# Kernel tuning notes

Hardware: AMD Instinct MI355X
Metric: run time of the kernel (lower is better)

Reference implementation:

```python
import jax, jax.numpy as jnp
import numpy as np

B, N, E = 256, 128, 262144
LABEL_DIM, MAX_DEGREE, RW_DIM = 29, 16, 16
F = 128
NUM_LABELS = LABEL_DIM + MAX_DEGREE + RW_DIM  # 61
SK_ITER, SK_TAU = 6, 1.0


def _edges(k):
    k1, k2, k3 = jax.random.split(k, 3)
    g = jax.random.randint(k1, (E,), 0, B)
    src = g * N + jax.random.randint(k2, (E,), 0, N)
    dst = g * N + jax.random.randint(k3, (E,), 0, N)
    return src, dst


def setup_inputs():
    key = jax.random.key(0)
    ks = jax.random.split(key, 20)
    ntot = B * N
    s = 0.05
    nrm = lambda k, shp: jax.random.normal(k, shp, dtype=jnp.float32) * s
    src1, dst1 = _edges(ks[3])
    src2, dst2 = _edges(ks[7])
    return {
        'x1': jax.random.uniform(ks[0], (ntot, LABEL_DIM), dtype=jnp.float32),
        'cent1': jax.random.randint(ks[1], (ntot,), 0, MAX_DEGREE),
        'rw1': jax.random.uniform(ks[2], (ntot, RW_DIM), dtype=jnp.float32),
        'src1': src1, 'dst1': dst1,
        'x2': jax.random.uniform(ks[4], (ntot, LABEL_DIM), dtype=jnp.float32),
        'cent2': jax.random.randint(ks[5], (ntot,), 0, MAX_DEGREE),
        'rw2': jax.random.uniform(ks[6], (ntot, RW_DIM), dtype=jnp.float32),
        'src2': src2, 'dst2': dst2,
        'degree_emb': nrm(ks[8], (MAX_DEGREE, MAX_DEGREE)),
        'init_W': nrm(ks[9], (NUM_LABELS, F)), 'init_b': jnp.zeros((F,), jnp.float32),
        'W1': nrm(ks[10], (F, F)), 'b1': jnp.zeros((F,), jnp.float32),
        'W2': nrm(ks[11], (F, F)), 'b2': jnp.zeros((F,), jnp.float32),
        'W3': nrm(ks[12], (F, F)), 'b3': jnp.zeros((F,), jnp.float32),
        'A_aff': nrm(ks[13], (F, F)) + jnp.eye(F, dtype=jnp.float32),
        'sc_W1': nrm(ks[14], (8 * F, 64)), 'sc_b1': jnp.zeros((64,), jnp.float32),
        'sc_W2': nrm(ks[15], (64, 1)), 'sc_b2': jnp.zeros((1,), jnp.float32),
        'topk': 8,
    }


def gcn_conv(x, W, b, src, dst):
    # GCNConv: x' = D^{-1/2} (A + I) D^{-1/2} x W + b
    n = x.shape[0]
    h = x @ W
    loops = jnp.arange(n)
    s = jnp.concatenate([src, loops])
    d = jnp.concatenate([dst, loops])
    deg = jax.ops.segment_sum(jnp.ones_like(d, dtype=h.dtype), d, n)
    dinv = jax.lax.rsqrt(jnp.maximum(deg, 1.0))
    w = dinv[s] * dinv[d]
    return jax.ops.segment_sum(h[s] * w[:, None], d, n) + b


def conv_pass(feat, src, dst, W1, b1, W2, b2, W3, b3):
    f1 = gcn_conv(feat, W1, b1, src, dst)
    f2 = gcn_conv(jax.nn.relu(f1), W2, b2, src, dst)
    f3 = gcn_conv(jax.nn.relu(f2), W3, b3, src, dst)
    return f1, f2, f3


def affinity(xa, xb, A):
    Xa = xa.reshape(B, N, -1)
    Xb = xb.reshape(B, N, -1)
    return jnp.einsum('bif,fg,bjg->bij', Xa, A, Xb)


def soft_topk(scores, ks_tgt, n_iter, tau):
    # Entropic-OT soft top-k (Xie et al.) over flattened affinity entries vs 2 anchors,
    # normalized by SK_ITER log-domain Sinkhorn iterations.
    b, n, m = scores.shape
    L = n * m
    x = scores.reshape(b, L)
    a_lo = x.min(axis=1, keepdims=True) - 1.0
    a_hi = x.max(axis=1, keepdims=True) + 1.0
    anchors = jnp.concatenate([a_lo, a_hi], axis=1)      # [b, 2]
    logK = -jnp.abs(x[:, :, None] - anchors[:, None, :]) / tau  # [b, L, 2]
    log_mu = jnp.full((b, L), -jnp.log(float(L)), dtype=x.dtype)
    k = ks_tgt[:, None]
    nu = jnp.concatenate([(L - k) / L, k / L], axis=1)   # [b, 2]
    log_nu = jnp.log(nu)

    def body(carry, _):
        f, g = carry
        f = log_mu - jax.nn.logsumexp(logK + g[:, None, :], axis=2)
        g = log_nu - jax.nn.logsumexp(logK + f[:, :, None], axis=1)
        return (f, g), None

    init = (jnp.zeros((b, L), x.dtype), jnp.zeros((b, 2), x.dtype))
    (f, g), _ = jax.lax.scan(body, init, None, length=n_iter)
    gamma = jnp.exp(logK + f[:, :, None] + g[:, None, :])
    prob = (gamma[:, :, 1] * L).reshape(b, n, m)
    return gamma, prob


def reference(x1, cent1, rw1, src1, dst1, x2, cent2, rw2, src2, dst2,
              degree_emb, init_W, init_b, W1, b1, W2, b2, W3, b3, A_aff,
              sc_W1, sc_b1, sc_W2, sc_b2, topk):
    feat1 = jax.nn.relu(jnp.concatenate([x1, degree_emb[cent1], rw1], axis=1) @ init_W + init_b)
    feat2 = jax.nn.relu(jnp.concatenate([x2, degree_emb[cent2], rw2], axis=1) @ init_W + init_b)
    f11, f12, f13 = conv_pass(feat1, src1, dst1, W1, b1, W2, b2, W3, b3)
    f21, f22, f23 = conv_pass(feat2, src2, dst2, W1, b1, W2, b2, W3, b3)

    gt_ks = jnp.full((B,), topk / 2.0, dtype=feat1.dtype)
    _, sim1 = soft_topk(affinity(feat1, feat2, A_aff), gt_ks, SK_ITER, SK_TAU)
    _, sim2 = soft_topk(affinity(f13, f23, A_aff), gt_ks, SK_ITER, SK_TAU)

    gf1 = jnp.concatenate([feat1, f11, f12, f13], axis=1).reshape(B, N, -1).sum(axis=1)   # global_add_pool
    gf2 = jnp.concatenate([feat2, f21, f22, f23], axis=1).reshape(B, N, -1).max(axis=1)   # global_max_pool
    scores = jnp.concatenate([gf1, gf2], axis=1)  # [B, 8F]
    h = jax.nn.relu(scores @ sc_W1 + sc_b1)
    ged = jax.nn.sigmoid((h @ sc_W2 + sc_b2).reshape(-1))
    return ged, sim1, sim2
```

## Files before the change

kernel.cpp:

```cpp
#include <hip/hip_runtime.h>
#include <math.h>

#define BATCH 256
#define NNODE 128
#define NT    32768
#define FDIM  128
#define NEDGE 262144
#define LBL   29
#define MAXDEG 16
#define RWD   16
#define NTF   (NT * FDIM)

__global__ void k_zero2(int* __restrict__ p1, int* __restrict__ p2) {
  int i = blockIdx.x * 256 + threadIdx.x;
  if (i < NT) p1[i] = 0;
  else if (i < 2 * NT) p2[i - NT] = 0;
}
__global__ void k_deg2(const int* __restrict__ dst1, const int* __restrict__ dst2,
                       int* __restrict__ d1, int* __restrict__ d2) {
  int e = blockIdx.x * 256 + threadIdx.x;
  if (e < NEDGE) atomicAdd(&d1[dst1[e]], 1);
  else if (e < 2 * NEDGE) atomicAdd(&d2[dst2[e - NEDGE]], 1);
}
__global__ void k_dinv2(const int* __restrict__ d1, const int* __restrict__ d2,
                        float* __restrict__ v1, float* __restrict__ v2) {
  int i = blockIdx.x * 256 + threadIdx.x;
  if (i < NT) v1[i] = rsqrtf((float)(d1[i] + 1));
  else if (i < 2 * NT) v2[i - NT] = rsqrtf((float)(d2[i - NT] + 1));
}
__global__ __launch_bounds__(1024) void k_scan2(const int* __restrict__ degi1,
                                                int* __restrict__ ofs1, int* __restrict__ cur1,
                                                const int* __restrict__ degi2,
                                                int* __restrict__ ofs2, int* __restrict__ cur2) {
  const int* degi = blockIdx.x ? degi2 : degi1;
  int* ofs = blockIdx.x ? ofs2 : ofs1;
  int* cur = blockIdx.x ? cur2 : cur1;
  __shared__ int part[1024];
  int t = threadIdx.x;
  int base = t * 32;
  int loc[32]; int sum = 0;
#pragma unroll
  for (int u = 0; u < 32; ++u) { loc[u] = sum; sum += degi[base + u]; }
  part[t] = sum;
  __syncthreads();
  for (int off = 1; off < 1024; off <<= 1) {
    int v = (t >= off) ? part[t - off] : 0;
    __syncthreads();
    part[t] += v;
    __syncthreads();
  }
  int excl = (t == 0) ? 0 : part[t - 1];
#pragma unroll
  for (int u = 0; u < 32; ++u) {
    int o = excl + loc[u];
    ofs[base + u] = o; cur[base + u] = o;
  }
}
__global__ void k_fill2(const int* __restrict__ src1, const int* __restrict__ dst1,
                        int* __restrict__ cur1, int* __restrict__ csr1,
                        const int* __restrict__ src2, const int* __restrict__ dst2,
                        int* __restrict__ cur2, int* __restrict__ csr2) {
  int e = blockIdx.x * 256 + threadIdx.x;
  if (e < NEDGE) {
    int pos = atomicAdd(&cur1[dst1[e]], 1);
    csr1[pos] = src1[e];
  } else if (e < 2 * NEDGE) {
    e -= NEDGE;
    int pos = atomicAdd(&cur2[dst2[e]], 1);
    csr2[pos] = src2[e];
  }
}

__global__ __launch_bounds__(256, 2) void k_chain(
    const float* __restrict__ x1, const int* __restrict__ cent1, const float* __restrict__ rw1,
    const float* __restrict__ x2, const int* __restrict__ cent2, const float* __restrict__ rw2,
    const float* __restrict__ demb,
    const float* __restrict__ initW, const float* __restrict__ initb,
    const float* __restrict__ W1, const float* __restrict__ b1,
    const float* __restrict__ W2, const float* __restrict__ b2,
    const float* __restrict__ W3, const float* __restrict__ b3,
    const int* __restrict__ ofs1, const int* __restrict__ end1, const int* __restrict__ csr1,
    const int* __restrict__ ofs2, const int* __restrict__ end2, const int* __restrict__ csr2,
    const float* __restrict__ dinv1, const float* __restrict__ dinv2,
    float* __restrict__ feat1G, float* __restrict__ feat2G,
    float* __restrict__ f13G, float* __restrict__ f23G,
    float* __restrict__ gfs) {
  __shared__ float X[128 * 132];
  __shared__ float WcB[16 * 132];
  __shared__ float dvL[128];
  __shared__ float bL[128];
  __shared__ int   oL[128], enL[128];

  const int t = threadIdx.x;
  const int side = blockIdx.x >> 8;
  const int g = blockIdx.x & 255;
  const int nb = g * NNODE;

  const float* xg    = side ? x2 : x1;
  const int*   centg = side ? cent2 : cent1;
  const float* rwg   = side ? rw2 : rw1;
  const int*   ofsg  = side ? ofs2 : ofs1;
  const int*   endg  = side ? end2 : end1;
  const int*   csrg  = side ? csr2 : csr1;
  const float* dinvg = side ? dinv2 : dinv1;
  float* featG = side ? feat2G : feat1G;
  float* f3G   = side ? f23G : f13G;

  const int e_base = ofsg[nb];
  if (t < 128) {
    dvL[t] = dinvg[nb + t];
    oL[t]  = ofsg[nb + t] - e_base;
    enL[t] = endg[nb + t] - e_base;
  }
  {
    int d = t >> 1, sub = t & 1;
    int node = nb + d;
    int ct = centg[node];
    const float* xr = xg + (size_t)node * LBL;
    const float* er = demb + ct * MAXDEG;
    const float* rr = rwg + (size_t)node * RWD;
    for (int c = sub * 34; c < sub * 34 + 34; ++c) {
      float v = 0.f;
      if (c < LBL) v = xr[c];
      else if (c < LBL + MAXDEG) v = er[c - LBL];
      else if (c < 61) v = rr[c - 45];
      X[d * 68 + c] = v;
    }
  }
  __syncthreads();

  const int rg = t >> 3;
  const int jq = (t & 7) * 4;

  {
    float acc[4][16] = {};
    for (int kc = 0; kc < 64; kc += 16) {
      __syncthreads();
#pragma unroll
      for (int u = 0; u < 2; ++u) {
        int ll = t + 256 * u;
        int row = ll >> 5, c4 = (ll & 31) * 4;
        int gk = kc + row;
        float4 w = (gk < 61) ? *reinterpret_cast<const float4*>(&initW[(size_t)gk * FDIM + c4])
                             : make_float4(0.f, 0.f, 0.f, 0.f);
        *reinterpret_cast<float4*>(&WcB[row * 132 + c4]) = w;
      }
      if (kc == 0 && t < 128) bL[t] = initb[t];
      __syncthreads();
      for (int kk = 0; kk < 16; kk += 4) {
        float av[4][4];
#pragma unroll
        for (int r = 0; r < 4; ++r) {
          float4 tmp = *reinterpret_cast<const float4*>(&X[(rg + 32 * r) * 68 + kc + kk]);
          av[r][0] = tmp.x; av[r][1] = tmp.y; av[r][2] = tmp.z; av[r][3] = tmp.w;
        }
#pragma unroll
        for (int c = 0; c < 4; ++c) {
          float4 w0 = *reinterpret_cast<const float4*>(&WcB[(kk + c) * 132 + jq]);
          float4 w1 = *reinterpret_cast<const float4*>(&WcB[(kk + c) * 132 + 32 + jq]);
          float4 w2 = *reinterpret_cast<const float4*>(&WcB[(kk + c) * 132 + 64 + jq]);
          float4 w3 = *reinterpret_cast<const float4*>(&WcB[(kk + c) * 132 + 96 + jq]);
#pragma unroll
          for (int r = 0; r < 4; ++r) {
            float a = av[r][c];
            acc[r][0]  += a * w0.x; acc[r][1]  += a * w0.y; acc[r][2]  += a * w0.z; acc[r][3]  += a * w0.w;
            acc[r][4]  += a * w1.x; acc[r][5]  += a * w1.y; acc[r][6]  += a * w1.z; acc[r][7]  += a * w1.w;
            acc[r][8]  += a * w2.x; acc[r][9]  += a * w2.y; acc[r][10] += a * w2.z; acc[r][11] += a * w2.w;
            acc[r][12] += a * w3.x; acc[r][13] += a * w3.y; acc[r][14] += a * w3.z; acc[r][15] += a * w3.w;
          }
        }
      }
    }
    __syncthreads();
#pragma unroll
    for (int r = 0; r < 4; ++r) {
      int row = rg + 32 * r;
#pragma unroll
      for (int q = 0; q < 4; ++q) {
        int col = q * 32 + jq;
        float4 bl = *reinterpret_cast<const float4*>(&bL[col]);
        float4 o = make_float4(fmaxf(acc[r][q * 4 + 0] + bl.x, 0.f),
                               fmaxf(acc[r][q * 4 + 1] + bl.y, 0.f),
                               fmaxf(acc[r][q * 4 + 2] + bl.z, 0.f),
                               fmaxf(acc[r][q * 4 + 3] + bl.w, 0.f));
        *reinterpret_cast<float4*>(&X[row * 132 + col]) = o;
        *reinterpret_cast<float4*>(&featG[(size_t)(nb + row) * FDIM + col]) = o;
      }
    }
    __syncthreads();
  }

#define POOL_LAYER(layer)                                                            \
  {                                                                                  \
    int j4 = (t & 31) * 4, qq = t >> 5;                                              \
    float4 pv = side ? make_float4(-INFINITY, -INFINITY, -INFINITY, -INFINITY)       \
                     : make_float4(0.f, 0.f, 0.f, 0.f);                              \
    for (int r = 0; r < 16; ++r) {                                                   \
      float4 fv = *reinterpret_cast<const float4*>(&X[(qq * 16 + r) * 132 + j4]);    \
      if (side) { pv.x = fmaxf(pv.x, fv.x); pv.y = fmaxf(pv.y, fv.y);                \
                  pv.z = fmaxf(pv.z, fv.z); pv.w = fmaxf(pv.w, fv.w); }              \
      else      { pv.x += fv.x; pv.y += fv.y; pv.z += fv.z; pv.w += fv.w; }          \
    }                                                                                \
    *reinterpret_cast<float4*>(&WcB[qq * 128 + j4]) = pv;                            \
    __syncthreads();                                                                 \
    if (t < 128) {                                                                   \
      float v = side ? -INFINITY : 0.f;                                              \
      for (int q2 = 0; q2 < 8; ++q2) {                                               \
        float w2 = WcB[q2 * 128 + t];                                                \
        v = side ? fmaxf(v, w2) : (v + w2);                                          \
      }                                                                              \
      gfs[g * 1024 + side * 512 + (layer) * 128 + t] = v;                            \
    }                                                                                \
  }

  POOL_LAYER(0)

  for (int l = 0; l < 3; ++l) {
    const float* Wg = (l == 0) ? W1 : (l == 1) ? W2 : W3;
    const float* bg = (l == 0) ? b1 : (l == 1) ? b2 : b3;
    float acc[4][16] = {};
    for (int kc = 0; kc < 128; kc += 16) {
      __syncthreads();
#pragma unroll
      for (int u = 0; u < 2; ++u) {
        int ll = t + 256 * u;
        int row = ll >> 5, c4 = (ll & 31) * 4;
        *reinterpret_cast<float4*>(&WcB[row * 132 + c4]) =
            *reinterpret_cast<const float4*>(&Wg[(size_t)(kc + row) * FDIM + c4]);
      }
      if (kc == 0 && t < 128) bL[t] = bg[t];
      __syncthreads();
      for (int kk = 0; kk < 16; kk += 4) {
        float av[4][4];
#pragma unroll
        for (int r = 0; r < 4; ++r) {
          float4 tmp = *reinterpret_cast<const float4*>(&X[(rg + 32 * r) * 132 + kc + kk]);
          if (l > 0) {
            tmp.x = fmaxf(tmp.x, 0.f); tmp.y = fmaxf(tmp.y, 0.f);
            tmp.z = fmaxf(tmp.z, 0.f); tmp.w = fmaxf(tmp.w, 0.f);
          }
          av[r][0] = tmp.x; av[r][1] = tmp.y; av[r][2] = tmp.z; av[r][3] = tmp.w;
        }
#pragma unroll
        for (int c = 0; c < 4; ++c) {
          float4 w0 = *reinterpret_cast<const float4*>(&WcB[(kk + c) * 132 + jq]);
          float4 w1 = *reinterpret_cast<const float4*>(&WcB[(kk + c) * 132 + 32 + jq]);
          float4 w2 = *reinterpret_cast<const float4*>(&WcB[(kk + c) * 132 + 64 + jq]);
          float4 w3 = *reinterpret_cast<const float4*>(&WcB[(kk + c) * 132 + 96 + jq]);
#pragma unroll
          for (int r = 0; r < 4; ++r) {
            float a = av[r][c];
            acc[r][0]  += a * w0.x; acc[r][1]  += a * w0.y; acc[r][2]  += a * w0.z; acc[r][3]  += a * w0.w;
            acc[r][4]  += a * w1.x; acc[r][5]  += a * w1.y; acc[r][6]  += a * w1.z; acc[r][7]  += a * w1.w;
            acc[r][8]  += a * w2.x; acc[r][9]  += a * w2.y; acc[r][10] += a * w2.z; acc[r][11] += a * w2.w;
            acc[r][12] += a * w3.x; acc[r][13] += a * w3.y; acc[r][14] += a * w3.z; acc[r][15] += a * w3.w;
          }
        }
      }
    }
    __syncthreads();
#pragma unroll
    for (int r = 0; r < 4; ++r) {
      int row = rg + 32 * r;
#pragma unroll
      for (int q = 0; q < 4; ++q) {
        int col = q * 32 + jq;
        *reinterpret_cast<float4*>(&X[row * 132 + col]) =
            make_float4(acc[r][q * 4 + 0], acc[r][q * 4 + 1],
                        acc[r][q * 4 + 2], acc[r][q * 4 + 3]);
      }
    }
    __syncthreads();

    {
      int d = t >> 1, fc = (t & 1) * 64;
      float dd = dvL[d];
      float4 a[16];
#pragma unroll
      for (int u = 0; u < 16; ++u) {
        float4 hv = *reinterpret_cast<const float4*>(&X[d * 132 + fc + u * 4]);
        a[u] = make_float4(dd * hv.x, dd * hv.y, dd * hv.z, dd * hv.w);
      }
      int o0 = oL[d], o1 = enL[d];
      int sj = (o0 < o1) ? (csrg[e_base + o0] - nb) : 0;
      for (int j = o0; j < o1; ++j) {
        int sn = (j + 1 < o1) ? (csrg[e_base + j + 1] - nb) : 0;
        float w = dvL[sj];
#pragma unroll
        for (int u = 0; u < 16; ++u) {
          float4 hv = *reinterpret_cast<const float4*>(&X[sj * 132 + fc + u * 4]);
          a[u].x += w * hv.x; a[u].y += w * hv.y; a[u].z += w * hv.z; a[u].w += w * hv.w;
        }
        sj = sn;
      }
      __syncthreads();
#pragma unroll
      for (int u = 0; u < 16; ++u) {
        float4 bl = *reinterpret_cast<const float4*>(&bL[fc + u * 4]);
        float4 o = make_float4(bl.x + dd * a[u].x, bl.y + dd * a[u].y,
                               bl.z + dd * a[u].z, bl.w + dd * a[u].w);
        *reinterpret_cast<float4*>(&X[d * 132 + fc + u * 4]) = o;
        if (l == 2)
          *reinterpret_cast<float4*>(&f3G[(size_t)(nb + d) * FDIM + fc + u * 4]) = o;
      }
    }
    __syncthreads();

    POOL_LAYER(l + 1)
  }
#undef POOL_LAYER
}

__global__ __launch_bounds__(1024) void k_sim(const float* __restrict__ F1,
                                              const float* __restrict__ F2,
                                              const float* __restrict__ Aaff,
                                              const int* __restrict__ topk,
                                              float* __restrict__ Sout) {
  __shared__ float X1[128 * 132];
  __shared__ float X2[128 * 132];
  __shared__ float WcB[16 * 132];
  __shared__ float rA[16], rB[16], bc[2];

  const int t = threadIdx.x;
  const int b = blockIdx.x;
  const float* F1b = F1 + (size_t)b * NNODE * FDIM;
  const float* F2b = F2 + (size_t)b * NNODE * FDIM;

#pragma unroll
  for (int p = 0; p < 4; ++p) {
    int fi = t + 1024 * p;
    int row = fi >> 5, c4 = (fi & 31) * 4;
    *reinterpret_cast<float4*>(&X1[row * 132 + c4]) =
        *reinterpret_cast<const float4*>(&F1b[(size_t)row * FDIM + c4]);
    *reinterpret_cast<float4*>(&X2[row * 132 + c4]) =
        *reinterpret_cast<const float4*>(&F2b[(size_t)row * FDIM + c4]);
  }

  const int rg = t >> 3;
  const int jq = (t & 7) * 4;

  float acc[16];
#pragma unroll
  for (int u = 0; u < 16; ++u) acc[u] = 0.f;

  for (int kc = 0; kc < 128; kc += 16) {
    __syncthreads();
    if (t < 512) {
      int row = t >> 5, c4 = (t & 31) * 4;
      *reinterpret_cast<float4*>(&WcB[row * 132 + c4]) =
          *reinterpret_cast<const float4*>(&Aaff[(size_t)(kc + row) * FDIM + c4]);
    }
    __syncthreads();
    for (int kk = 0; kk < 16; kk += 4) {
      float4 a4 = *reinterpret_cast<const float4*>(&X1[rg * 132 + kc + kk]);
      float av[4] = {a4.x, a4.y, a4.z, a4.w};
#pragma unroll
      for (int c = 0; c < 4; ++c) {
        float4 w0 = *reinterpret_cast<const float4*>(&WcB[(kk + c) * 132 + jq]);
        float4 w1 = *reinterpret_cast<const float4*>(&WcB[(kk + c) * 132 + 32 + jq]);
        float4 w2 = *reinterpret_cast<const float4*>(&WcB[(kk + c) * 132 + 64 + jq]);
        float4 w3 = *reinterpret_cast<const float4*>(&WcB[(kk + c) * 132 + 96 + jq]);
        float a = av[c];
        acc[0]  += a * w0.x; acc[1]  += a * w0.y; acc[2]  += a * w0.z; acc[3]  += a * w0.w;
        acc[4]  += a * w1.x; acc[5]  += a * w1.y; acc[6]  += a * w1.z; acc[7]  += a * w1.w;
        acc[8]  += a * w2.x; acc[9]  += a * w2.y; acc[10] += a * w2.z; acc[11] += a * w2.w;
        acc[12] += a * w3.x; acc[13] += a * w3.y; acc[14] += a * w3.z; acc[15] += a * w3.w;
      }
    }
  }
  __syncthreads();
#pragma unroll
  for (int q = 0; q < 4; ++q)
    *reinterpret_cast<float4*>(&X1[rg * 132 + 32 * q + jq]) =
        make_float4(acc[q * 4 + 0], acc[q * 4 + 1], acc[q * 4 + 2], acc[q * 4 + 3]);

#pragma unroll
  for (int u = 0; u < 16; ++u) acc[u] = 0.f;

  for (int kc = 0; kc < 128; kc += 16) {
    __syncthreads();
#pragma unroll
    for (int p = 0; p < 2; ++p) {
      int id = t + 1024 * p;
      int kkr = id >> 7, c = id & 127;
      WcB[kkr * 132 + c] = X2[c * 132 + kc + kkr];
    }
    __syncthreads();
    for (int kk = 0; kk < 16; kk += 4) {
      float4 a4 = *reinterpret_cast<const float4*>(&X1[rg * 132 + kc + kk]);
      float av[4] = {a4.x, a4.y, a4.z, a4.w};
#pragma unroll
      for (int c = 0; c < 4; ++c) {
        float4 w0 = *reinterpret_cast<const float4*>(&WcB[(kk + c) * 132 + jq]);
        float4 w1 = *reinterpret_cast<const float4*>(&WcB[(kk + c) * 132 + 32 + jq]);
        float4 w2 = *reinterpret_cast<const float4*>(&WcB[(kk + c) * 132 + 64 + jq]);
        float4 w3 = *reinterpret_cast<const float4*>(&WcB[(kk + c) * 132 + 96 + jq]);
        float a = av[c];
        acc[0]  += a * w0.x; acc[1]  += a * w0.y; acc[2]  += a * w0.z; acc[3]  += a * w0.w;
        acc[4]  += a * w1.x; acc[5]  += a * w1.y; acc[6]  += a * w1.z; acc[7]  += a * w1.w;
        acc[8]  += a * w2.x; acc[9]  += a * w2.y; acc[10] += a * w2.z; acc[11] += a * w2.w;
        acc[12] += a * w3.x; acc[13] += a * w3.y; acc[14] += a * w3.z; acc[15] += a * w3.w;
      }
    }
  }

  const int wave = t >> 6, lane = t & 63;
  {
    float mn = acc[0], mx = acc[0];
#pragma unroll
    for (int u = 1; u < 16; ++u) { mn = fminf(mn, acc[u]); mx = fmaxf(mx, acc[u]); }
    for (int off = 32; off; off >>= 1) {
      mn = fminf(mn, __shfl_down(mn, off));
      mx = fmaxf(mx, __shfl_down(mx, off));
    }
    if (lane == 0) { rA[wave] = mn; rB[wave] = mx; }
    __syncthreads();
    if (t < 16) {
      mn = rA[t]; mx = rB[t];
      for (int off = 8; off; off >>= 1) {
        mn = fminf(mn, __shfl_down(mn, off));
        mx = fmaxf(mx, __shfl_down(mx, off));
      }
      if (t == 0) { bc[0] = mn - 1.f; bc[1] = mx + 1.f; }
    }
    __syncthreads();
  }
  float a_lo = bc[0], a_hi = bc[1];

  float p[16], q[16];
#pragma unroll
  for (int u = 0; u < 16; ++u) {
    p[u] = __expf(a_lo - acc[u]);
    q[u] = __expf(acc[u] - a_hi);
  }

  const float Lf = (float)(NNODE * NNODE);
  float kt = 0.5f * (float)topk[0];

  float E0 = 1.f, E1 = 1.f, E0p = 1.f, E1p = 1.f;
  for (int it = 0; it < 6; ++it) {
    E0p = E0; E1p = E1;
    float r0 = 0.f, r1 = 0.f;
#pragma unroll
    for (int u = 0; u < 16; ++u) {
      float denom = fmaf(p[u], E0, q[u] * E1);
      float rin = __builtin_amdgcn_rcpf(denom);
      r0 = fmaf(p[u], rin, r0);
      r1 = fmaf(q[u], rin, r1);
    }
    for (int off = 32; off; off >>= 1) {
      r0 += __shfl_down(r0, off);
      r1 += __shfl_down(r1, off);
    }
    if (lane == 0) { rA[wave] = r0; rB[wave] = r1; }
    __syncthreads();
    if (t < 16) {
      r0 = rA[t]; r1 = rB[t];
      for (int off = 8; off; off >>= 1) {
        r0 += __shfl_down(r0, off);
        r1 += __shfl_down(r1, off);
      }
      if (t == 0) { bc[0] = (Lf - kt) / r0; bc[1] = kt / r1; }
    }
    __syncthreads();
    E0 = bc[0]; E1 = bc[1];
    __syncthreads();
  }

  float* xrow = Sout + (size_t)b * NNODE * NNODE + (size_t)rg * NNODE;
#pragma unroll
  for (int qd = 0; qd < 4; ++qd) {
    float o[4];
#pragma unroll
    for (int j = 0; j < 4; ++j) {
      int u = qd * 4 + j;
      float denom = fmaf(p[u], E0p, q[u] * E1p);
      o[j] = q[u] * E1 * __builtin_amdgcn_rcpf(denom);
    }
    *reinterpret_cast<float4*>(&xrow[32 * qd + jq]) = make_float4(o[0], o[1], o[2], o[3]);
  }
}

__global__ __launch_bounds__(256) void k_mlp(const float* __restrict__ gfs,
                                             const float* __restrict__ W1,
                                             const float* __restrict__ b1,
                                             const float* __restrict__ W2,
                                             const float* __restrict__ b2,
                                             float* __restrict__ ged) {
  __shared__ float sm[1024];
  int b = blockIdx.x, t = threadIdx.x;
  const float* s = gfs + b * 1024;
#pragma unroll
  for (int qq = 0; qq < 4; ++qq) sm[t + 256 * qq] = s[t + 256 * qq];
  __syncthreads();
  int j4 = (t & 15) * 4, kp = t >> 4;
  float4 acc = make_float4(0.f, 0.f, 0.f, 0.f);
#pragma unroll 8
  for (int k = 0; k < 64; ++k) {
    float4 w = *reinterpret_cast<const float4*>(&W1[(size_t)(kp * 64 + k) * 64 + j4]);
    float sv = sm[kp * 64 + k];
    acc.x += sv * w.x; acc.y += sv * w.y; acc.z += sv * w.z; acc.w += sv * w.w;
  }
  __syncthreads();
  *reinterpret_cast<float4*>(&sm[kp * 64 + j4]) = acc;
  __syncthreads();
  if (t < 64) {
    float h = b1[t];
#pragma unroll
    for (int kp2 = 0; kp2 < 16; ++kp2) h += sm[kp2 * 64 + t];
    h = fmaxf(h, 0.f);
    float v = h * W2[t];
    for (int off = 32; off; off >>= 1) v += __shfl_down(v, off);
    if (t == 0) ged[b] = 1.f / (1.f + __expf(-(v + b2[0])));
  }
}

extern "C" void kernel_launch(void* const* d_in, const int* in_sizes, int n_in,
                              void* d_out, int out_size, void* d_ws, size_t ws_size,
                              hipStream_t stream) {
  (void)in_sizes; (void)n_in; (void)out_size; (void)ws_size;
  const float* x1    = (const float*)d_in[0];
  const int*   cent1 = (const int*)  d_in[1];
  const float* rw1   = (const float*)d_in[2];
  const int*   src1  = (const int*)  d_in[3];
  const int*   dst1  = (const int*)  d_in[4];
  const float* x2    = (const float*)d_in[5];
  const int*   cent2 = (const int*)  d_in[6];
  const float* rw2   = (const float*)d_in[7];
  const int*   src2  = (const int*)  d_in[8];
  const int*   dst2  = (const int*)  d_in[9];
  const float* demb  = (const float*)d_in[10];
  const float* initW = (const float*)d_in[11];
  const float* initb = (const float*)d_in[12];
  const float* W1    = (const float*)d_in[13];
  const float* b1    = (const float*)d_in[14];
  const float* W2    = (const float*)d_in[15];
  const float* b2    = (const float*)d_in[16];
  const float* W3    = (const float*)d_in[17];
  const float* b3    = (const float*)d_in[18];
  const float* Aaff  = (const float*)d_in[19];
  const float* scW1  = (const float*)d_in[20];
  const float* scb1  = (const float*)d_in[21];
  const float* scW2  = (const float*)d_in[22];
  const float* scb2  = (const float*)d_in[23];
  const int*   topk  = (const int*)  d_in[24];

  float* ws    = (float*)d_ws;
  float* feat1 = ws;
  float* feat2 = ws + (size_t)1 * NTF;
  float* f13   = ws + (size_t)2 * NTF;
  float* f23   = ws + (size_t)3 * NTF;
  float* dinv1 = ws + (size_t)4 * NTF;
  float* dinv2 = dinv1 + NT;
  float* gfs   = dinv2 + NT;

  float* ged = (float*)d_out;
  float* S1  = ged + BATCH;
  float* S2  = S1 + (size_t)BATCH * NNODE * NNODE;

  int* degi1 = (int*)S1;
  int* ofs1  = degi1 + NT;
  int* cur1  = ofs1 + NT;
  int* csr1  = cur1 + NT;
  int* degi2 = csr1 + NEDGE;
  int* ofs2  = degi2 + NT;
  int* cur2  = ofs2 + NT;
  int* csr2  = cur2 + NT;

  const int gE = NEDGE / 256;
  const int gN = NT / 256;

  k_zero2<<<2 * gN, 256, 0, stream>>>(degi1, degi2);
  k_deg2<<<2 * gE, 256, 0, stream>>>(dst1, dst2, degi1, degi2);
  k_dinv2<<<2 * gN, 256, 0, stream>>>(degi1, degi2, dinv1, dinv2);
  k_scan2<<<2, 1024, 0, stream>>>(degi1, ofs1, cur1, degi2, ofs2, cur2);
  k_fill2<<<2 * gE, 256, 0, stream>>>(src1, dst1, cur1, csr1, src2, dst2, cur2, csr2);

  k_chain<<<512, 256, 0, stream>>>(
      x1, cent1, rw1, x2, cent2, rw2, demb, initW, initb,
      W1, b1, W2, b2, W3, b3,
      ofs1, cur1, csr1, ofs2, cur2, csr2, dinv1, dinv2,
      feat1, feat2, f13, f23, gfs);

  k_mlp<<<BATCH, 256, 0, stream>>>(gfs, scW1, scb1, scW2, scb2, ged);

  k_sim<<<BATCH, 1024, 0, stream>>>(feat1, feat2, Aaff, topk, S1);
  k_sim<<<BATCH, 1024, 0, stream>>>(f13, f23, Aaff, topk, S2);
}
```

Baseline: 455.5 us.

## Prefetch weights into registers, merge sim launches, transpose X2 once, fuse dinv into scan

Register-prefetches the next weight tile in the chain and sim GEMM loops so global loads overlap the current tile's compute. The two k_sim launches become one 512-block launch. X2 is stored transposed with a rotated column offset at load time, which removes the per-tile transpose into WcB and its two barriers. The dinv computation moves into the scan kernel and the zero kernel becomes hipMemsetAsync, cutting launches at the cost of a slightly heavier single-block scan.

```diff
diff --git a/kernel.cpp b/kernel.cpp
--- a/kernel.cpp
+++ b/kernel.cpp
@@ -11,36 +11,32 @@
 #define RWD   16
 #define NTF   (NT * FDIM)
 
-__global__ void k_zero2(int* __restrict__ p1, int* __restrict__ p2) {
-  int i = blockIdx.x * 256 + threadIdx.x;
-  if (i < NT) p1[i] = 0;
-  else if (i < 2 * NT) p2[i - NT] = 0;
-}
 __global__ void k_deg2(const int* __restrict__ dst1, const int* __restrict__ dst2,
                        int* __restrict__ d1, int* __restrict__ d2) {
   int e = blockIdx.x * 256 + threadIdx.x;
   if (e < NEDGE) atomicAdd(&d1[dst1[e]], 1);
   else if (e < 2 * NEDGE) atomicAdd(&d2[dst2[e - NEDGE]], 1);
 }
-__global__ void k_dinv2(const int* __restrict__ d1, const int* __restrict__ d2,
-                        float* __restrict__ v1, float* __restrict__ v2) {
-  int i = blockIdx.x * 256 + threadIdx.x;
-  if (i < NT) v1[i] = rsqrtf((float)(d1[i] + 1));
-  else if (i < 2 * NT) v2[i - NT] = rsqrtf((float)(d2[i - NT] + 1));
-}
 __global__ __launch_bounds__(1024) void k_scan2(const int* __restrict__ degi1,
                                                 int* __restrict__ ofs1, int* __restrict__ cur1,
+                                                float* __restrict__ dinv1,
                                                 const int* __restrict__ degi2,
-                                                int* __restrict__ ofs2, int* __restrict__ cur2) {
+                                                int* __restrict__ ofs2, int* __restrict__ cur2,
+                                                float* __restrict__ dinv2) {
   const int* degi = blockIdx.x ? degi2 : degi1;
-  int* ofs = blockIdx.x ? ofs2 : ofs1;
-  int* cur = blockIdx.x ? cur2 : cur1;
+  int* ofs   = blockIdx.x ? ofs2  : ofs1;
+  int* cur   = blockIdx.x ? cur2  : cur1;
+  float* dnv = blockIdx.x ? dinv2 : dinv1;
   __shared__ int part[1024];
   int t = threadIdx.x;
   int base = t * 32;
   int loc[32]; int sum = 0;
 #pragma unroll
-  for (int u = 0; u < 32; ++u) { loc[u] = sum; sum += degi[base + u]; }
+  for (int u = 0; u < 32; ++u) {
+    int dg = degi[base + u];
+    loc[u] = sum; sum += dg;
+    dnv[base + u] = rsqrtf((float)(dg + 1));
+  }
   part[t] = sum;
   __syncthreads();
   for (int off = 1; off < 1024; off <<= 1) {
@@ -131,21 +127,32 @@
 
   const int rg = t >> 3;
   const int jq = (t & 7) * 4;
+  const int prow = t >> 5;
+  const int pc4  = (t & 31) * 4;
 
   {
     float acc[4][16] = {};
+    float4 wpre[2];
+#pragma unroll
+    for (int u = 0; u < 2; ++u) {
+      int gk = prow + 8 * u;
+      wpre[u] = (gk < 61) ? *reinterpret_cast<const float4*>(&initW[(size_t)gk * FDIM + pc4])
+                          : make_float4(0.f, 0.f, 0.f, 0.f);
+    }
     for (int kc = 0; kc < 64; kc += 16) {
       __syncthreads();
 #pragma unroll
-      for (int u = 0; u < 2; ++u) {
-        int ll = t + 256 * u;
-        int row = ll >> 5, c4 = (ll & 31) * 4;
-        int gk = kc + row;
-        float4 w = (gk < 61) ? *reinterpret_cast<const float4*>(&initW[(size_t)gk * FDIM + c4])
-                             : make_float4(0.f, 0.f, 0.f, 0.f);
-        *reinterpret_cast<float4*>(&WcB[row * 132 + c4]) = w;
-      }
+      for (int u = 0; u < 2; ++u)
+        *reinterpret_cast<float4*>(&WcB[(prow + 8 * u) * 132 + pc4]) = wpre[u];
       if (kc == 0 && t < 128) bL[t] = initb[t];
+      if (kc + 16 < 64) {
+#pragma unroll
+        for (int u = 0; u < 2; ++u) {
+          int gk = kc + 16 + prow + 8 * u;
+          wpre[u] = (gk < 61) ? *reinterpret_cast<const float4*>(&initW[(size_t)gk * FDIM + pc4])
+                              : make_float4(0.f, 0.f, 0.f, 0.f);
+        }
+      }
       __syncthreads();
       for (int kk = 0; kk < 16; kk += 4) {
         float av[4][4];
@@ -219,16 +226,21 @@
     const float* Wg = (l == 0) ? W1 : (l == 1) ? W2 : W3;
     const float* bg = (l == 0) ? b1 : (l == 1) ? b2 : b3;
     float acc[4][16] = {};
+    float4 wpre[2];
+#pragma unroll
+    for (int u = 0; u < 2; ++u)
+      wpre[u] = *reinterpret_cast<const float4*>(&Wg[(size_t)(prow + 8 * u) * FDIM + pc4]);
     for (int kc = 0; kc < 128; kc += 16) {
       __syncthreads();
 #pragma unroll
-      for (int u = 0; u < 2; ++u) {
-        int ll = t + 256 * u;
-        int row = ll >> 5, c4 = (ll & 31) * 4;
-        *reinterpret_cast<float4*>(&WcB[row * 132 + c4]) =
-            *reinterpret_cast<const float4*>(&Wg[(size_t)(kc + row) * FDIM + c4]);
-      }
+      for (int u = 0; u < 2; ++u)
+        *reinterpret_cast<float4*>(&WcB[(prow + 8 * u) * 132 + pc4]) = wpre[u];
       if (kc == 0 && t < 128) bL[t] = bg[t];
+      if (kc + 16 < 128) {
+#pragma unroll
+        for (int u = 0; u < 2; ++u)
+          wpre[u] = *reinterpret_cast<const float4*>(&Wg[(size_t)(kc + 16 + prow + 8 * u) * FDIM + pc4]);
+      }
       __syncthreads();
       for (int kk = 0; kk < 16; kk += 4) {
         float av[4][4];
@@ -311,20 +323,25 @@
 #undef POOL_LAYER
 }
 
-__global__ __launch_bounds__(1024) void k_sim(const float* __restrict__ F1,
-                                              const float* __restrict__ F2,
+__global__ __launch_bounds__(1024) void k_sim(const float* __restrict__ F1s1,
+                                              const float* __restrict__ F2s1,
+                                              const float* __restrict__ F1s2,
+                                              const float* __restrict__ F2s2,
                                               const float* __restrict__ Aaff,
                                               const int* __restrict__ topk,
-                                              float* __restrict__ Sout) {
+                                              float* __restrict__ S1,
+                                              float* __restrict__ S2) {
   __shared__ float X1[128 * 132];
   __shared__ float X2[128 * 132];
   __shared__ float WcB[16 * 132];
   __shared__ float rA[16], rB[16], bc[2];
 
   const int t = threadIdx.x;
-  const int b = blockIdx.x;
-  const float* F1b = F1 + (size_t)b * NNODE * FDIM;
-  const float* F2b = F2 + (size_t)b * NNODE * FDIM;
+  const int half = blockIdx.x >> 8;
+  const int b = blockIdx.x & 255;
+  const float* F1b = (half ? F1s2 : F1s1) + (size_t)b * NNODE * FDIM;
+  const float* F2b = (half ? F2s2 : F2s1) + (size_t)b * NNODE * FDIM;
+  float* Sout = (half ? S2 : S1) + (size_t)b * NNODE * NNODE;
 
 #pragma unroll
   for (int p = 0; p < 4; ++p) {
@@ -332,8 +349,12 @@
     int row = fi >> 5, c4 = (fi & 31) * 4;
     *reinterpret_cast<float4*>(&X1[row * 132 + c4]) =
         *reinterpret_cast<const float4*>(&F1b[(size_t)row * FDIM + c4]);
-    *reinterpret_cast<float4*>(&X2[row * 132 + c4]) =
-        *reinterpret_cast<const float4*>(&F2b[(size_t)row * FDIM + c4]);
+    float4 v = *reinterpret_cast<const float4*>(&F2b[(size_t)row * FDIM + c4]);
+    int ro = (row + c4) & 127;
+    X2[(c4 + 0) * 132 + ro] = v.x;
+    X2[(c4 + 1) * 132 + ro] = v.y;
+    X2[(c4 + 2) * 132 + ro] = v.z;
+    X2[(c4 + 3) * 132 + ro] = v.w;
   }
 
   const int rg = t >> 3;
@@ -343,12 +364,18 @@
 #pragma unroll
   for (int u = 0; u < 16; ++u) acc[u] = 0.f;
 
+  float4 apre;
+  if (t < 512) {
+    int row = t >> 5, c4 = (t & 31) * 4;
+    apre = *reinterpret_cast<const float4*>(&Aaff[(size_t)row * FDIM + c4]);
+  }
   for (int kc = 0; kc < 128; kc += 16) {
     __syncthreads();
     if (t < 512) {
       int row = t >> 5, c4 = (t & 31) * 4;
-      *reinterpret_cast<float4*>(&WcB[row * 132 + c4]) =
-          *reinterpret_cast<const float4*>(&Aaff[(size_t)(kc + row) * FDIM + c4]);
+      *reinterpret_cast<float4*>(&WcB[row * 132 + c4]) = apre;
+      if (kc + 16 < 128)
+        apre = *reinterpret_cast<const float4*>(&Aaff[(size_t)(kc + 16 + row) * FDIM + c4]);
     }
     __syncthreads();
     for (int kk = 0; kk < 16; kk += 4) {
@@ -376,25 +403,21 @@
 
 #pragma unroll
   for (int u = 0; u < 16; ++u) acc[u] = 0.f;
+  __syncthreads();
 
   for (int kc = 0; kc < 128; kc += 16) {
-    __syncthreads();
-#pragma unroll
-    for (int p = 0; p < 2; ++p) {
-      int id = t + 1024 * p;
-      int kkr = id >> 7, c = id & 127;
-      WcB[kkr * 132 + c] = X2[c * 132 + kc + kkr];
-    }
-    __syncthreads();
     for (int kk = 0; kk < 16; kk += 4) {
       float4 a4 = *reinterpret_cast<const float4*>(&X1[rg * 132 + kc + kk]);
       float av[4] = {a4.x, a4.y, a4.z, a4.w};
 #pragma unroll
       for (int c = 0; c < 4; ++c) {
-        float4 w0 = *reinterpret_cast<const float4*>(&WcB[(kk + c) * 132 + jq]);
-        float4 w1 = *reinterpret_cast<const float4*>(&WcB[(kk + c) * 132 + 32 + jq]);
-        float4 w2 = *reinterpret_cast<const float4*>(&WcB[(kk + c) * 132 + 64 + jq]);
-        float4 w3 = *reinterpret_cast<const float4*>(&WcB[(kk + c) * 132 + 96 + jq]);
+        int ck = kc + kk + c;
+        const float* xb = &X2[ck * 132];
+        int o0 = (jq + (ck & 124)) & 127;
+        float4 w0 = *reinterpret_cast<const float4*>(&xb[o0]);
+        float4 w1 = *reinterpret_cast<const float4*>(&xb[(o0 + 32) & 127]);
+        float4 w2 = *reinterpret_cast<const float4*>(&xb[(o0 + 64) & 127]);
+        float4 w3 = *reinterpret_cast<const float4*>(&xb[(o0 + 96) & 127]);
         float a = av[c];
         acc[0]  += a * w0.x; acc[1]  += a * w0.y; acc[2]  += a * w0.z; acc[3]  += a * w0.w;
         acc[4]  += a * w1.x; acc[5]  += a * w1.y; acc[6]  += a * w1.z; acc[7]  += a * w1.w;
@@ -467,7 +490,7 @@
     __syncthreads();
   }
 
-  float* xrow = Sout + (size_t)b * NNODE * NNODE + (size_t)rg * NNODE;
+  float* xrow = Sout + (size_t)rg * NNODE;
 #pragma unroll
   for (int qd = 0; qd < 4; ++qd) {
     float o[4];
@@ -568,12 +591,11 @@
   int* csr2  = cur2 + NT;
 
   const int gE = NEDGE / 256;
-  const int gN = NT / 256;
-
-  k_zero2<<<2 * gN, 256, 0, stream>>>(degi1, degi2);
+
+  hipMemsetAsync(degi1, 0, NT * sizeof(int), stream);
+  hipMemsetAsync(degi2, 0, NT * sizeof(int), stream);
   k_deg2<<<2 * gE, 256, 0, stream>>>(dst1, dst2, degi1, degi2);
-  k_dinv2<<<2 * gN, 256, 0, stream>>>(degi1, degi2, dinv1, dinv2);
-  k_scan2<<<2, 1024, 0, stream>>>(degi1, ofs1, cur1, degi2, ofs2, cur2);
+  k_scan2<<<2, 1024, 0, stream>>>(degi1, ofs1, cur1, dinv1, degi2, ofs2, cur2, dinv2);
   k_fill2<<<2 * gE, 256, 0, stream>>>(src1, dst1, cur1, csr1, src2, dst2, cur2, csr2);
 
   k_chain<<<512, 256, 0, stream>>>(
@@ -584,6 +606,5 @@
 
   k_mlp<<<BATCH, 256, 0, stream>>>(gfs, scW1, scb1, scW2, scb2, ged);
 
-  k_sim<<<BATCH, 1024, 0, stream>>>(feat1, feat2, Aaff, topk, S1);
-  k_sim<<<BATCH, 1024, 0, stream>>>(f13, f23, Aaff, topk, S2);
+  k_sim<<<512, 1024, 0, stream>>>(feat1, feat2, f13, f23, Aaff, topk, S1, S2);
 }
```

Result: slower. 468.2 us (+2.8%).
